# Kernel optimization log

Measured on AMD Instinct MI355X. Metric: run time of the kernel, lower is better.

Reference implementation:

```python
import jax, jax.numpy as jnp
import numpy as np

T, H, E, F, K, FS = 2048, 2048, 64, 512, 8, 512


def setup_inputs() -> dict:
    key = jax.random.key(0)
    ks = jax.random.split(key, 6)
    s = 0.02
    return {
        "hidden_states": jax.random.normal(ks[0], (T, H), jnp.float32),
        # merged gate: E router logits + 1 shared-expert gate logit
        "W_gate": jax.random.normal(ks[1], (H, E + 1), jnp.float32) * s,
        # per-expert merged gate_up proj: [E, H, 2F]
        "W_gate_up": jax.random.normal(ks[2], (E, H, 2 * F), jnp.float32) * s,
        "W_down": jax.random.normal(ks[3], (E, F, H), jnp.float32) * s,
        # shared expert
        "Ws_gate_up": jax.random.normal(ks[4], (H, 2 * FS), jnp.float32) * s,
        "Ws_down": jax.random.normal(ks[5], (FS, H), jnp.float32) * s,
    }


def reference(hidden_states, W_gate, W_gate_up, W_down, Ws_gate_up, Ws_down):
    x = hidden_states  # [T, H]
    logits_all = x @ W_gate                      # [T, E+1]
    router_logits = logits_all[:, :E]
    shared_gate_logit = logits_all[:, E:]        # [T, 1]

    # FusedMoE routing: softmax -> top_k -> renormalize (norm_topk_prob=True)
    probs = jax.nn.softmax(router_logits.astype(jnp.float32), axis=-1)
    topk_w, topk_idx = jax.lax.top_k(probs, K)   # [T, K]
    topk_w = topk_w / jnp.sum(topk_w, axis=-1, keepdims=True)
    # dense combine weights [T, E] (zero for unselected experts)
    combine = jnp.zeros((T, E), probs.dtype).at[
        jnp.arange(T)[:, None], topk_idx].set(topk_w)

    # grouped expert GEMMs (dense reference: every expert sees all tokens,
    # combine-weights zero-out unrouted pairs)
    gu = jnp.einsum('th,ehf->etf', x, W_gate_up)   # [E, T, 2F]
    g, u = jnp.split(gu, 2, axis=-1)
    act = jax.nn.silu(g) * u                       # [E, T, F]
    # apply combine weight before down-proj to avoid [E, T, H] intermediate
    act = act * combine.T[:, :, None].astype(act.dtype)
    routed = jnp.einsum('etf,efh->th', act, W_down)  # [T, H]

    # shared expert (Qwen3NextMLP with sigmoid expert_gate)
    sgu = x @ Ws_gate_up                           # [T, 2FS]
    sg, su = jnp.split(sgu, 2, axis=-1)
    shared = (jax.nn.silu(sg) * su) @ Ws_down      # [T, H]
    shared = jax.nn.sigmoid(shared_gate_logit) * shared

    return shared + routed.astype(x.dtype)
```

## Files before the change

### kernel.cpp

```cpp
#include <hip/hip_runtime.h>
#include <hip/hip_bf16.h>
#include <math.h>

#define T_TOK 2048
#define H_DIM 2048
#define E_NUM 64
#define F_DIM 512
#define K_TOP 8
#define FS_DIM 512
#define NROWS (T_TOK * K_TOP)

typedef __attribute__((ext_vector_type(8))) short short8v;
typedef __attribute__((ext_vector_type(4))) float f32x4;

static __device__ __forceinline__ unsigned short f2bf(float f) {
    unsigned int u = __float_as_uint(f);
    u += 0x7fff + ((u >> 16) & 1);
    return (unsigned short)(u >> 16);
}

#define BCHUNK(row, k8) ((((k8) ^ ((row) + ((row) >> 3)))) & 7)
#define ASWZ(row) (((row) + ((row) >> 3)) & 7)

typedef const unsigned int __attribute__((address_space(1))) gu32;
typedef unsigned int __attribute__((address_space(3))) lu32;
#define GLDS16(gsrc, ldst) \
    __builtin_amdgcn_global_load_lds((gu32*)(gsrc), (lu32*)(ldst), 16, 0, 0)

__global__ __launch_bounds__(256) void cvt_bf16_kernel(
    const float* __restrict__ in, unsigned short* __restrict__ out, int n8)
{
    int i = blockIdx.x * 256 + threadIdx.x;
    if (i < n8) {
        const float4* p = (const float4*)(in + (size_t)i * 8);
        float4 v0 = p[0], v1 = p[1];
        ushort4 a = make_ushort4(f2bf(v0.x), f2bf(v0.y), f2bf(v0.z), f2bf(v0.w));
        ushort4 b = make_ushort4(f2bf(v1.x), f2bf(v1.y), f2bf(v1.z), f2bf(v1.w));
        ushort4* q = (ushort4*)(out + (size_t)i * 8);
        q[0] = a; q[1] = b;
    }
}

__global__ __launch_bounds__(64) void router_kernel(
    const float* __restrict__ x, const float* __restrict__ Wg,
    int* __restrict__ topk_idx, float* __restrict__ topk_w,
    float* __restrict__ sgate, int* __restrict__ counts)
{
    const int t = blockIdx.x;
    const int lane = threadIdx.x;
    const float* xr = x + (size_t)t * H_DIM;

    float a0 = 0.f, a1 = 0.f, a2 = 0.f, a3 = 0.f;
    for (int h = 0; h < H_DIM; h += 4) {
        float4 xv = *(const float4*)&xr[h];
        a0 += xv.x * Wg[(h + 0) * 65 + lane];
        a1 += xv.y * Wg[(h + 1) * 65 + lane];
        a2 += xv.z * Wg[(h + 2) * 65 + lane];
        a3 += xv.w * Wg[(h + 3) * 65 + lane];
    }
    float logit = (a0 + a1) + (a2 + a3);

    float a64 = 0.f;
    for (int h = lane; h < H_DIM; h += 64) a64 += xr[h] * Wg[h * 65 + 64];
#pragma unroll
    for (int off = 32; off >= 1; off >>= 1) a64 += __shfl_xor(a64, off);

    float v = logit;
    float selv[K_TOP]; int seli[K_TOP];
#pragma unroll
    for (int k = 0; k < K_TOP; ++k) {
        float mv = v; int mi = lane;
#pragma unroll
        for (int off = 32; off >= 1; off >>= 1) {
            float ov = __shfl_xor(mv, off);
            int   oi = __shfl_xor(mi, off);
            if (ov > mv || (ov == mv && oi < mi)) { mv = ov; mi = oi; }
        }
        selv[k] = mv; seli[k] = mi;
        if (lane == mi) v = -INFINITY;
    }

    if (lane == 0) {
        float m = selv[0];
        float w[K_TOP]; float s = 0.f;
#pragma unroll
        for (int k = 0; k < K_TOP; ++k) { w[k] = __expf(selv[k] - m); s += w[k]; }
        float inv = 1.f / s;
#pragma unroll
        for (int k = 0; k < K_TOP; ++k) {
            topk_idx[t * K_TOP + k] = seli[k];
            topk_w[t * K_TOP + k] = w[k] * inv;
            atomicAdd(&counts[seli[k]], 1);
        }
        sgate[t] = 1.f / (1.f + __expf(-a64));
    }
}

__global__ __launch_bounds__(256) void bucket_kernel(
    const int* __restrict__ topk_idx, const float* __restrict__ topk_w,
    const int* __restrict__ counts, int* __restrict__ offsets,
    int* __restrict__ bucket_tok, float* __restrict__ bucket_w)
{
    const int e = blockIdx.x, thr = threadIdx.x;
    __shared__ int cnt[256];
    __shared__ int base_s;
    const int q0 = thr * 64;
    int c = 0;
    for (int q = 0; q < 64; ++q) c += (topk_idx[q0 + q] == e) ? 1 : 0;
    cnt[thr] = c;
    __syncthreads();
    if (thr == 0) {
        int off = 0;
        for (int i = 0; i < e; ++i) off += counts[i];
        offsets[e] = off;
        base_s = off;
        int run = 0;
        for (int i = 0; i < 256; ++i) { int tval = cnt[i]; cnt[i] = run; run += tval; }
    }
    __syncthreads();
    int pos = base_s + cnt[thr];
    for (int q = 0; q < 64; ++q) {
        int pp = q0 + q;
        if (topk_idx[pp] == e) {
            bucket_tok[pos] = pp >> 3;
            bucket_w[pos] = topk_w[pp];
            ++pos;
        }
    }
}

template<bool ROUTED>
__global__ __launch_bounds__(512, 6) void gu_mfma_kernel(
    const unsigned short* __restrict__ xb,
    const float* __restrict__ Wall,
    const int* __restrict__ counts, const int* __restrict__ offsets,
    const int* __restrict__ bucket_tok, const float* __restrict__ bucket_w,
    unsigned short* __restrict__ actout)
{
    constexpr int BM = 256;
    __shared__ __align__(16) unsigned short As[BM * 64];
    __shared__ __align__(16) unsigned short Bs[64 * 64];
    __shared__ int   toksS[BM];
    __shared__ float twsS[BM];

    const int tid  = threadIdx.x;
    const int lane = tid & 63;
    const int wid  = tid >> 6;
    const int wm = wid >> 1, wn = wid & 1;
    const int lrow = lane & 15, lhi = lane >> 4;

    int cblk, mt, ne, base;
    const float* W;
    if (ROUTED) {
        int nw = (blockIdx.x & 7) * ((int)gridDim.x >> 3) + (blockIdx.x >> 3);
        int e = nw >> 5; mt = (nw >> 4) & 1; cblk = nw & 15;
        ne = counts[e]; base = offsets[e];
        if (mt * BM >= ne) return;
        W = Wall + (size_t)e * H_DIM * (2 * F_DIM);
    } else {
        cblk = blockIdx.x; mt = blockIdx.y;
        ne = T_TOK; base = 0;
        W = Wall;
    }
    const int c0 = cblk * 32;

    const int n4 = (tid & 15) * 4;
    const int kb = (tid >> 4) * 2;
    const int n5 = n4 & 31;
    const int wcol = ((n5 < 16) ? 0 : (F_DIM - 16)) + c0 + (n4 >> 5) * 16 + n5;
    int wr_off[4];
#pragma unroll
    for (int cc = 0; cc < 4; ++cc) {
        int n = n4 + cc;
        wr_off[cc] = n * 64 + BCHUNK(n, kb >> 3) * 8 + (kb & 7);
    }
    const int rg = wn * 32 + lrow, ru = wn * 32 + 16 + lrow;
    int rdBg[2], rdBu[2];
#pragma unroll
    for (int ks = 0; ks < 2; ++ks) {
        int kc = ks * 4 + lhi;
        rdBg[ks] = rg * 64 + BCHUNK(rg, kc) * 8;
        rdBu[ks] = ru * 64 + BCHUNK(ru, kc) * 8;
    }
    int rdA[4][2];
#pragma unroll
    for (int fm = 0; fm < 4; ++fm) {
        int arow = wm * 64 + fm * 16 + lrow;
#pragma unroll
        for (int ks = 0; ks < 2; ++ks) {
            int kc = ks * 4 + lhi;
            rdA[fm][ks] = arow * 64 + (((kc ^ ASWZ(arow)) & 7) << 3);
        }
    }
    const int m0_stride = ROUTED ? (2 * BM) : ((int)gridDim.y * BM);

    for (int m0 = mt * BM; m0 < ne; m0 += m0_stride) {
        __syncthreads();
        if (tid < BM) {
            int idx = m0 + tid; bool v = idx < ne;
            if (ROUTED) {
                toksS[tid] = v ? bucket_tok[base + idx] : bucket_tok[base];
                twsS[tid]  = v ? bucket_w[base + idx] : 0.f;
            } else {
                toksS[tid] = v ? idx : (T_TOK - 1);
                twsS[tid]  = 1.f;
            }
        }
        __syncthreads();

        int asrc[4];
#pragma unroll
        for (int i = 0; i < 4; ++i) {
            int row = wid * 32 + i * 8 + (lane >> 3);
            asrc[i] = toksS[row] * H_DIM + (((lane & 7) ^ ASWZ(row)) << 3);
        }

        f32x4 acc[4][2];
#pragma unroll
        for (int i = 0; i < 4; ++i) {
            acc[i][0] = (f32x4){0.f, 0.f, 0.f, 0.f};
            acc[i][1] = (f32x4){0.f, 0.f, 0.f, 0.f};
        }

        const int NT = H_DIM / 64;
        float4 b0 = *(const float4*)&W[(size_t)kb * (2 * F_DIM) + wcol];
        float4 b1 = *(const float4*)&W[(size_t)(kb + 1) * (2 * F_DIM) + wcol];

        for (int kt = 0; kt < NT; ++kt) {
            const int k0 = kt * 64;
            __syncthreads();
#pragma unroll
            for (int i = 0; i < 4; ++i)
                GLDS16(xb + asrc[i] + k0, &As[(wid * 32 + i * 8) * 64]);
#pragma unroll
            for (int cc = 0; cc < 4; ++cc)
                *(ushort2*)&Bs[wr_off[cc]] = make_ushort2(
                    f2bf(((const float*)&b0)[cc]), f2bf(((const float*)&b1)[cc]));
            {
                int knx = (kt + 1 < NT) ? (k0 + 64) : k0;
                b0 = *(const float4*)&W[(size_t)(knx + kb) * (2 * F_DIM) + wcol];
                b1 = *(const float4*)&W[(size_t)(knx + kb + 1) * (2 * F_DIM) + wcol];
            }
            __syncthreads();
#pragma unroll
            for (int ks = 0; ks < 2; ++ks) {
                short8v bg = *(const short8v*)&Bs[rdBg[ks]];
                short8v bu = *(const short8v*)&Bs[rdBu[ks]];
#pragma unroll
                for (int fm = 0; fm < 4; ++fm) {
                    short8v af = *(const short8v*)&As[rdA[fm][ks]];
                    acc[fm][0] = __builtin_amdgcn_mfma_f32_16x16x32_bf16(af, bg, acc[fm][0], 0, 0, 0);
                    acc[fm][1] = __builtin_amdgcn_mfma_f32_16x16x32_bf16(af, bu, acc[fm][1], 0, 0, 0);
                }
            }
        }

        const int acol = c0 + wn * 16 + lrow;
#pragma unroll
        for (int fm = 0; fm < 4; ++fm) {
#pragma unroll
            for (int i = 0; i < 4; ++i) {
                int ml = wm * 64 + fm * 16 + lhi * 4 + i;
                int idx = m0 + ml;
                if (idx < ne) {
                    float gv = acc[fm][0][i], uv = acc[fm][1][i];
                    float s = gv / (1.f + __expf(-gv));
                    float val = s * uv * twsS[ml];
                    size_t orow = ROUTED ? (size_t)(base + idx) : (size_t)idx;
                    actout[orow * F_DIM + acol] = f2bf(val);
                }
            }
        }
    }
}

template<bool ROUTED>
__global__ __launch_bounds__(512, 6) void down_mfma_kernel(
    const unsigned short* __restrict__ actb,
    const float* __restrict__ Wall,
    const int* __restrict__ counts, const int* __restrict__ offsets,
    const int* __restrict__ bucket_tok, const float* __restrict__ sgate,
    float* __restrict__ out)
{
    constexpr int BM = 256;
    __shared__ __align__(16) unsigned short As[BM * 64];
    __shared__ __align__(16) unsigned short Bs[64 * 64];
    __shared__ int   toksS[BM];
    __shared__ float sgS[BM];

    const int tid  = threadIdx.x;
    const int lane = tid & 63;
    const int wid  = tid >> 6;
    const int wm = wid >> 1, wn = wid & 1;
    const int lrow = lane & 15, lhi = lane >> 4;

    int cblk, mt, ne, base;
    const float* W;
    if (ROUTED) {
        int nw = (blockIdx.x & 7) * ((int)gridDim.x >> 3) + (blockIdx.x >> 3);
        int e = nw >> 6; mt = (nw >> 5) & 1; cblk = nw & 31;
        ne = counts[e]; base = offsets[e];
        if (mt * BM >= ne) return;
        W = Wall + (size_t)e * F_DIM * H_DIM;
    } else {
        cblk = blockIdx.x; mt = blockIdx.y;
        ne = T_TOK; base = 0;
        W = Wall;
    }
    const int c0 = cblk * 64;

    const int n4 = (tid & 15) * 4;
    const int kb = (tid >> 4) * 2;
    const int wcol = c0 + n4;
    int wr_off[4];
#pragma unroll
    for (int cc = 0; cc < 4; ++cc) {
        int n = n4 + cc;
        wr_off[cc] = n * 64 + BCHUNK(n, kb >> 3) * 8 + (kb & 7);
    }
    const int r0 = wn * 32 + lrow, r1 = wn * 32 + 16 + lrow;
    int rdB0[2], rdB1[2];
#pragma unroll
    for (int ks = 0; ks < 2; ++ks) {
        int kc = ks * 4 + lhi;
        rdB0[ks] = r0 * 64 + BCHUNK(r0, kc) * 8;
        rdB1[ks] = r1 * 64 + BCHUNK(r1, kc) * 8;
    }
    int rdA[4][2];
#pragma unroll
    for (int fm = 0; fm < 4; ++fm) {
        int arow = wm * 64 + fm * 16 + lrow;
#pragma unroll
        for (int ks = 0; ks < 2; ++ks) {
            int kc = ks * 4 + lhi;
            rdA[fm][ks] = arow * 64 + (((kc ^ ASWZ(arow)) & 7) << 3);
        }
    }
    const int m0_stride = ROUTED ? (2 * BM) : ((int)gridDim.y * BM);

    for (int m0 = mt * BM; m0 < ne; m0 += m0_stride) {
        __syncthreads();
        if (tid < BM) {
            int idx = m0 + tid;
            if (ROUTED) {
                toksS[tid] = (idx < ne) ? bucket_tok[base + idx] : 0;
            } else {
                sgS[tid] = sgate[(idx < ne) ? idx : (T_TOK - 1)];
            }
        }
        __syncthreads();

        int asrc[4];
#pragma unroll
        for (int i = 0; i < 4; ++i) {
            int row = wid * 32 + i * 8 + (lane >> 3);
            int grow = ROUTED ? min(base + m0 + row, NROWS - 1)
                              : min(m0 + row, T_TOK - 1);
            asrc[i] = grow * F_DIM + (((lane & 7) ^ ASWZ(row)) << 3);
        }

        f32x4 acc[4][2];
#pragma unroll
        for (int i = 0; i < 4; ++i) {
            acc[i][0] = (f32x4){0.f, 0.f, 0.f, 0.f};
            acc[i][1] = (f32x4){0.f, 0.f, 0.f, 0.f};
        }

        const int NT = F_DIM / 64;
        float4 b0 = *(const float4*)&W[(size_t)kb * H_DIM + wcol];
        float4 b1 = *(const float4*)&W[(size_t)(kb + 1) * H_DIM + wcol];

        for (int kt = 0; kt < NT; ++kt) {
            const int k0 = kt * 64;
            __syncthreads();
#pragma unroll
            for (int i = 0; i < 4; ++i)
                GLDS16(actb + asrc[i] + k0, &As[(wid * 32 + i * 8) * 64]);
#pragma unroll
            for (int cc = 0; cc < 4; ++cc)
                *(ushort2*)&Bs[wr_off[cc]] = make_ushort2(
                    f2bf(((const float*)&b0)[cc]), f2bf(((const float*)&b1)[cc]));
            {
                int knx = (kt + 1 < NT) ? (k0 + 64) : k0;
                b0 = *(const float4*)&W[(size_t)(knx + kb) * H_DIM + wcol];
                b1 = *(const float4*)&W[(size_t)(knx + kb + 1) * H_DIM + wcol];
            }
            __syncthreads();
#pragma unroll
            for (int ks = 0; ks < 2; ++ks) {
                short8v bf0 = *(const short8v*)&Bs[rdB0[ks]];
                short8v bf1 = *(const short8v*)&Bs[rdB1[ks]];
#pragma unroll
                for (int fm = 0; fm < 4; ++fm) {
                    short8v af = *(const short8v*)&As[rdA[fm][ks]];
                    acc[fm][0] = __builtin_amdgcn_mfma_f32_16x16x32_bf16(af, bf0, acc[fm][0], 0, 0, 0);
                    acc[fm][1] = __builtin_amdgcn_mfma_f32_16x16x32_bf16(af, bf1, acc[fm][1], 0, 0, 0);
                }
            }
        }

#pragma unroll
        for (int fm = 0; fm < 4; ++fm) {
#pragma unroll
            for (int fn = 0; fn < 2; ++fn) {
                int col = c0 + wn * 32 + fn * 16 + lrow;
#pragma unroll
                for (int i = 0; i < 4; ++i) {
                    int ml = wm * 64 + fm * 16 + lhi * 4 + i;
                    int idx = m0 + ml;
                    if (idx < ne) {
                        if (ROUTED) {
                            atomicAdd(&out[(size_t)toksS[ml] * H_DIM + col], acc[fm][fn][i]);
                        } else {
                            out[(size_t)idx * H_DIM + col] = sgS[ml] * acc[fm][fn][i];
                        }
                    }
                }
            }
        }
    }
}

extern "C" void kernel_launch(void* const* d_in, const int* in_sizes, int n_in,
                              void* d_out, int out_size, void* d_ws, size_t ws_size,
                              hipStream_t stream) {
    const float* x    = (const float*)d_in[0];
    const float* Wg   = (const float*)d_in[1];
    const float* Wgu  = (const float*)d_in[2];
    const float* Wd   = (const float*)d_in[3];
    const float* Wsgu = (const float*)d_in[4];
    const float* Wsd  = (const float*)d_in[5];
    float* out = (float*)d_out;

    char* p = (char*)d_ws;
    auto alloc = [&](size_t bytes) {
        char* r = p;
        p += (bytes + 255) & ~(size_t)255;
        return r;
    };
    int*   topk_idx   = (int*)  alloc((size_t)T_TOK * K_TOP * sizeof(int));
    float* topk_w     = (float*)alloc((size_t)T_TOK * K_TOP * sizeof(float));
    float* sgate      = (float*)alloc((size_t)T_TOK * sizeof(float));
    int*   counts     = (int*)  alloc((size_t)E_NUM * sizeof(int));
    int*   offsets    = (int*)  alloc((size_t)E_NUM * sizeof(int));
    int*   bucket_tok = (int*)  alloc((size_t)NROWS * sizeof(int));
    float* bucket_w   = (float*)alloc((size_t)NROWS * sizeof(float));
    unsigned short* xb    = (unsigned short*)alloc((size_t)T_TOK * H_DIM * sizeof(short));
    unsigned short* act_r = (unsigned short*)alloc((size_t)NROWS * F_DIM * sizeof(short));
    unsigned short* act_s = (unsigned short*)alloc((size_t)T_TOK * FS_DIM * sizeof(short));

    hipMemsetAsync(counts, 0, E_NUM * sizeof(int), stream);
    cvt_bf16_kernel<<<(T_TOK * H_DIM / 8 + 255) / 256, 256, 0, stream>>>(x, xb, T_TOK * H_DIM / 8);
    router_kernel<<<T_TOK, 64, 0, stream>>>(x, Wg, topk_idx, topk_w, sgate, counts);
    bucket_kernel<<<E_NUM, 256, 0, stream>>>(topk_idx, topk_w, counts, offsets, bucket_tok, bucket_w);

    gu_mfma_kernel<true><<<16 * E_NUM * 2, 512, 0, stream>>>(
        xb, Wgu, counts, offsets, bucket_tok, bucket_w, act_r);
    gu_mfma_kernel<false><<<dim3(16, T_TOK / 256), 512, 0, stream>>>(
        xb, Wsgu, counts, offsets, bucket_tok, bucket_w, act_s);

    down_mfma_kernel<false><<<dim3(32, T_TOK / 256), 512, 0, stream>>>(
        act_s, Wsd, counts, offsets, bucket_tok, sgate, out);
    down_mfma_kernel<true><<<32 * E_NUM * 2, 512, 0, stream>>>(
        act_r, Wd, counts, offsets, bucket_tok, sgate, out);
}
```

Before: 819.7 us.

## Double-buffer A and B LDS tiles in grouped MoE GEMMs with K-32 stages

Splits the K loop of both the gate-up and down MFMA kernels into 32-wide stages with ping-pong LDS buffers for A and B. The global-to-LDS load of the next stage is issued before the MFMAs of the current one, leaving one barrier per stage instead of two per 64-wide tile. The A tile swizzle changes to fit 32-column rows. This adds LDS use (A split in half but B doubled) and more barriers in total, which may affect occupancy.

```diff
diff --git a/kernel.cpp b/kernel.cpp
--- a/kernel.cpp
+++ b/kernel.cpp
@@ -20,7 +20,7 @@
 }
 
 #define BCHUNK(row, k8) ((((k8) ^ ((row) + ((row) >> 3)))) & 7)
-#define ASWZ(row) (((row) + ((row) >> 3)) & 7)
+#define ASW32(r) (((r) >> 1) & 3)
 
 typedef const unsigned int __attribute__((address_space(1))) gu32;
 typedef unsigned int __attribute__((address_space(3))) lu32;
@@ -138,8 +138,8 @@
     unsigned short* __restrict__ actout)
 {
     constexpr int BM = 256;
-    __shared__ __align__(16) unsigned short As[BM * 64];
-    __shared__ __align__(16) unsigned short Bs[64 * 64];
+    __shared__ __align__(16) unsigned short As[2][BM * 32];
+    __shared__ __align__(16) unsigned short Bs[2][64 * 64];
     __shared__ int   toksS[BM];
     __shared__ float twsS[BM];
 
@@ -182,16 +182,16 @@
         rdBg[ks] = rg * 64 + BCHUNK(rg, kc) * 8;
         rdBu[ks] = ru * 64 + BCHUNK(ru, kc) * 8;
     }
-    int rdA[4][2];
+    int rdA[4];
 #pragma unroll
     for (int fm = 0; fm < 4; ++fm) {
         int arow = wm * 64 + fm * 16 + lrow;
-#pragma unroll
-        for (int ks = 0; ks < 2; ++ks) {
-            int kc = ks * 4 + lhi;
-            rdA[fm][ks] = arow * 64 + (((kc ^ ASWZ(arow)) & 7) << 3);
-        }
-    }
+        rdA[fm] = arow * 32 + ((lhi ^ ASW32(arow)) << 3);
+    }
+    const int ar0 = wid * 32 + (lane >> 2);
+    const int ar1 = ar0 + 16;
+    const int NT   = H_DIM / 64;
+    const int SMAX = H_DIM / 32;
     const int m0_stride = ROUTED ? (2 * BM) : ((int)gridDim.y * BM);
 
     for (int m0 = mt * BM; m0 < ne; m0 += m0_stride) {
@@ -208,12 +208,8 @@
         }
         __syncthreads();
 
-        int asrc[4];
-#pragma unroll
-        for (int i = 0; i < 4; ++i) {
-            int row = wid * 32 + i * 8 + (lane >> 3);
-            asrc[i] = toksS[row] * H_DIM + (((lane & 7) ^ ASWZ(row)) << 3);
-        }
+        const int src0 = toksS[ar0] * H_DIM + (((lane & 3) ^ ASW32(ar0)) << 3);
+        const int src1 = toksS[ar1] * H_DIM + (((lane & 3) ^ ASW32(ar1)) << 3);
 
         f32x4 acc[4][2];
 #pragma unroll
@@ -222,37 +218,47 @@
             acc[i][1] = (f32x4){0.f, 0.f, 0.f, 0.f};
         }
 
-        const int NT = H_DIM / 64;
         float4 b0 = *(const float4*)&W[(size_t)kb * (2 * F_DIM) + wcol];
         float4 b1 = *(const float4*)&W[(size_t)(kb + 1) * (2 * F_DIM) + wcol];
-
-        for (int kt = 0; kt < NT; ++kt) {
-            const int k0 = kt * 64;
-            __syncthreads();
-#pragma unroll
-            for (int i = 0; i < 4; ++i)
-                GLDS16(xb + asrc[i] + k0, &As[(wid * 32 + i * 8) * 64]);
-#pragma unroll
-            for (int cc = 0; cc < 4; ++cc)
-                *(ushort2*)&Bs[wr_off[cc]] = make_ushort2(
-                    f2bf(((const float*)&b0)[cc]), f2bf(((const float*)&b1)[cc]));
-            {
-                int knx = (kt + 1 < NT) ? (k0 + 64) : k0;
+        GLDS16(xb + src0, &As[0][(wid * 32) * 32]);
+        GLDS16(xb + src1, &As[0][(wid * 32 + 16) * 32]);
+#pragma unroll
+        for (int cc = 0; cc < 4; ++cc)
+            *(ushort2*)&Bs[0][wr_off[cc]] = make_ushort2(
+                f2bf(((const float*)&b0)[cc]), f2bf(((const float*)&b1)[cc]));
+        b0 = *(const float4*)&W[(size_t)(64 + kb) * (2 * F_DIM) + wcol];
+        b1 = *(const float4*)&W[(size_t)(64 + kb + 1) * (2 * F_DIM) + wcol];
+        __syncthreads();
+
+        for (int s = 0; s < SMAX; ++s) {
+            const int kt = s >> 1;
+            if (s + 1 < SMAX) {
+                const int kof = (s + 1) * 32;
+                GLDS16(xb + src0 + kof, &As[(s + 1) & 1][(wid * 32) * 32]);
+                GLDS16(xb + src1 + kof, &As[(s + 1) & 1][(wid * 32 + 16) * 32]);
+            }
+            if ((s & 1) && (kt + 1 < NT)) {
+#pragma unroll
+                for (int cc = 0; cc < 4; ++cc)
+                    *(ushort2*)&Bs[(kt + 1) & 1][wr_off[cc]] = make_ushort2(
+                        f2bf(((const float*)&b0)[cc]), f2bf(((const float*)&b1)[cc]));
+                int knx = (kt + 2 < NT) ? (kt + 2) * 64 : (NT - 1) * 64;
                 b0 = *(const float4*)&W[(size_t)(knx + kb) * (2 * F_DIM) + wcol];
                 b1 = *(const float4*)&W[(size_t)(knx + kb + 1) * (2 * F_DIM) + wcol];
             }
+            __builtin_amdgcn_sched_barrier(0);
+            const unsigned short* A_ = As[s & 1];
+            const unsigned short* B_ = Bs[kt & 1];
+            const int ks = s & 1;
+            short8v bg = *(const short8v*)&B_[rdBg[ks]];
+            short8v bu = *(const short8v*)&B_[rdBu[ks]];
+#pragma unroll
+            for (int fm = 0; fm < 4; ++fm) {
+                short8v af = *(const short8v*)&A_[rdA[fm]];
+                acc[fm][0] = __builtin_amdgcn_mfma_f32_16x16x32_bf16(af, bg, acc[fm][0], 0, 0, 0);
+                acc[fm][1] = __builtin_amdgcn_mfma_f32_16x16x32_bf16(af, bu, acc[fm][1], 0, 0, 0);
+            }
             __syncthreads();
-#pragma unroll
-            for (int ks = 0; ks < 2; ++ks) {
-                short8v bg = *(const short8v*)&Bs[rdBg[ks]];
-                short8v bu = *(const short8v*)&Bs[rdBu[ks]];
-#pragma unroll
-                for (int fm = 0; fm < 4; ++fm) {
-                    short8v af = *(const short8v*)&As[rdA[fm][ks]];
-                    acc[fm][0] = __builtin_amdgcn_mfma_f32_16x16x32_bf16(af, bg, acc[fm][0], 0, 0, 0);
-                    acc[fm][1] = __builtin_amdgcn_mfma_f32_16x16x32_bf16(af, bu, acc[fm][1], 0, 0, 0);
-                }
-            }
         }
 
         const int acol = c0 + wn * 16 + lrow;
@@ -283,8 +289,8 @@
     float* __restrict__ out)
 {
     constexpr int BM = 256;
-    __shared__ __align__(16) unsigned short As[BM * 64];
-    __shared__ __align__(16) unsigned short Bs[64 * 64];
+    __shared__ __align__(16) unsigned short As[2][BM * 32];
+    __shared__ __align__(16) unsigned short Bs[2][64 * 64];
     __shared__ int   toksS[BM];
     __shared__ float sgS[BM];
 
@@ -326,16 +332,16 @@
         rdB0[ks] = r0 * 64 + BCHUNK(r0, kc) * 8;
         rdB1[ks] = r1 * 64 + BCHUNK(r1, kc) * 8;
     }
-    int rdA[4][2];
+    int rdA[4];
 #pragma unroll
     for (int fm = 0; fm < 4; ++fm) {
         int arow = wm * 64 + fm * 16 + lrow;
-#pragma unroll
-        for (int ks = 0; ks < 2; ++ks) {
-            int kc = ks * 4 + lhi;
-            rdA[fm][ks] = arow * 64 + (((kc ^ ASWZ(arow)) & 7) << 3);
-        }
-    }
+        rdA[fm] = arow * 32 + ((lhi ^ ASW32(arow)) << 3);
+    }
+    const int ar0 = wid * 32 + (lane >> 2);
+    const int ar1 = ar0 + 16;
+    const int NT   = F_DIM / 64;
+    const int SMAX = F_DIM / 32;
     const int m0_stride = ROUTED ? (2 * BM) : ((int)gridDim.y * BM);
 
     for (int m0 = mt * BM; m0 < ne; m0 += m0_stride) {
@@ -350,14 +356,10 @@
         }
         __syncthreads();
 
-        int asrc[4];
-#pragma unroll
-        for (int i = 0; i < 4; ++i) {
-            int row = wid * 32 + i * 8 + (lane >> 3);
-            int grow = ROUTED ? min(base + m0 + row, NROWS - 1)
-                              : min(m0 + row, T_TOK - 1);
-            asrc[i] = grow * F_DIM + (((lane & 7) ^ ASWZ(row)) << 3);
-        }
+        int g0 = ROUTED ? min(base + m0 + ar0, NROWS - 1) : min(m0 + ar0, T_TOK - 1);
+        int g1 = ROUTED ? min(base + m0 + ar1, NROWS - 1) : min(m0 + ar1, T_TOK - 1);
+        const int src0 = g0 * F_DIM + (((lane & 3) ^ ASW32(ar0)) << 3);
+        const int src1 = g1 * F_DIM + (((lane & 3) ^ ASW32(ar1)) << 3);
 
         f32x4 acc[4][2];
 #pragma unroll
@@ -366,37 +368,47 @@
             acc[i][1] = (f32x4){0.f, 0.f, 0.f, 0.f};
         }
 
-        const int NT = F_DIM / 64;
         float4 b0 = *(const float4*)&W[(size_t)kb * H_DIM + wcol];
         float4 b1 = *(const float4*)&W[(size_t)(kb + 1) * H_DIM + wcol];
-
-        for (int kt = 0; kt < NT; ++kt) {
-            const int k0 = kt * 64;
-            __syncthreads();
-#pragma unroll
-            for (int i = 0; i < 4; ++i)
-                GLDS16(actb + asrc[i] + k0, &As[(wid * 32 + i * 8) * 64]);
-#pragma unroll
-            for (int cc = 0; cc < 4; ++cc)
-                *(ushort2*)&Bs[wr_off[cc]] = make_ushort2(
-                    f2bf(((const float*)&b0)[cc]), f2bf(((const float*)&b1)[cc]));
-            {
-                int knx = (kt + 1 < NT) ? (k0 + 64) : k0;
+        GLDS16(actb + src0, &As[0][(wid * 32) * 32]);
+        GLDS16(actb + src1, &As[0][(wid * 32 + 16) * 32]);
+#pragma unroll
+        for (int cc = 0; cc < 4; ++cc)
+            *(ushort2*)&Bs[0][wr_off[cc]] = make_ushort2(
+                f2bf(((const float*)&b0)[cc]), f2bf(((const float*)&b1)[cc]));
+        b0 = *(const float4*)&W[(size_t)(64 + kb) * H_DIM + wcol];
+        b1 = *(const float4*)&W[(size_t)(64 + kb + 1) * H_DIM + wcol];
+        __syncthreads();
+
+        for (int s = 0; s < SMAX; ++s) {
+            const int kt = s >> 1;
+            if (s + 1 < SMAX) {
+                const int kof = (s + 1) * 32;
+                GLDS16(actb + src0 + kof, &As[(s + 1) & 1][(wid * 32) * 32]);
+                GLDS16(actb + src1 + kof, &As[(s + 1) & 1][(wid * 32 + 16) * 32]);
+            }
+            if ((s & 1) && (kt + 1 < NT)) {
+#pragma unroll
+                for (int cc = 0; cc < 4; ++cc)
+                    *(ushort2*)&Bs[(kt + 1) & 1][wr_off[cc]] = make_ushort2(
+                        f2bf(((const float*)&b0)[cc]), f2bf(((const float*)&b1)[cc]));
+                int knx = (kt + 2 < NT) ? (kt + 2) * 64 : (NT - 1) * 64;
                 b0 = *(const float4*)&W[(size_t)(knx + kb) * H_DIM + wcol];
                 b1 = *(const float4*)&W[(size_t)(knx + kb + 1) * H_DIM + wcol];
             }
+            __builtin_amdgcn_sched_barrier(0);
+            const unsigned short* A_ = As[s & 1];
+            const unsigned short* B_ = Bs[kt & 1];
+            const int ks = s & 1;
+            short8v bf0 = *(const short8v*)&B_[rdB0[ks]];
+            short8v bf1 = *(const short8v*)&B_[rdB1[ks]];
+#pragma unroll
+            for (int fm = 0; fm < 4; ++fm) {
+                short8v af = *(const short8v*)&A_[rdA[fm]];
+                acc[fm][0] = __builtin_amdgcn_mfma_f32_16x16x32_bf16(af, bf0, acc[fm][0], 0, 0, 0);
+                acc[fm][1] = __builtin_amdgcn_mfma_f32_16x16x32_bf16(af, bf1, acc[fm][1], 0, 0, 0);
+            }
             __syncthreads();
-#pragma unroll
-            for (int ks = 0; ks < 2; ++ks) {
-                short8v bf0 = *(const short8v*)&Bs[rdB0[ks]];
-                short8v bf1 = *(const short8v*)&Bs[rdB1[ks]];
-#pragma unroll
-                for (int fm = 0; fm < 4; ++fm) {
-                    short8v af = *(const short8v*)&As[rdA[fm][ks]];
-                    acc[fm][0] = __builtin_amdgcn_mfma_f32_16x16x32_bf16(af, bf0, acc[fm][0], 0, 0, 0);
-                    acc[fm][1] = __builtin_amdgcn_mfma_f32_16x16x32_bf16(af, bf1, acc[fm][1], 0, 0, 0);
-                }
-            }
         }
 
 #pragma unroll
```

Measured after the change: 745.4 us. 9.1% less time.

## Load A fragments directly from global and double-buffer B tile in LDS

Applied to the files above, without the earlier changes.

The A operand (tokens/activations) no longer goes through LDS via global_load_lds; each lane loads its MFMA fragments straight from global memory into registers, prefetched one half-step ahead. The B weight tile becomes double-buffered in LDS so one barrier per k-step suffices, and launch bounds drop occupancy to 4 waves/SIMD. The routed grids also stop splitting experts into two M-tiles, so each block loops over all of its expert's rows. This targets barrier stalls and LDS traffic, at the cost of uncoalesced 16-byte gathers of A, less parallelism for experts with many tokens, and reordered launch of the shared gate-up kernel.

```diff
diff --git a/kernel.cpp b/kernel.cpp
--- a/kernel.cpp
+++ b/kernel.cpp
@@ -20,12 +20,11 @@
 }
 
 #define BCHUNK(row, k8) ((((k8) ^ ((row) + ((row) >> 3)))) & 7)
-#define ASWZ(row) (((row) + ((row) >> 3)) & 7)
-
-typedef const unsigned int __attribute__((address_space(1))) gu32;
-typedef unsigned int __attribute__((address_space(3))) lu32;
-#define GLDS16(gsrc, ldst) \
-    __builtin_amdgcn_global_load_lds((gu32*)(gsrc), (lu32*)(ldst), 16, 0, 0)
+
+#define PIPE_BARRIER() do { \
+    asm volatile("s_waitcnt lgkmcnt(0)" ::: "memory"); \
+    __builtin_amdgcn_s_barrier(); \
+} while (0)
 
 __global__ __launch_bounds__(256) void cvt_bf16_kernel(
     const float* __restrict__ in, unsigned short* __restrict__ out, int n8)
@@ -130,7 +129,7 @@
 }
 
 template<bool ROUTED>
-__global__ __launch_bounds__(512, 6) void gu_mfma_kernel(
+__global__ __launch_bounds__(512, 4) void gu_mfma_kernel(
     const unsigned short* __restrict__ xb,
     const float* __restrict__ Wall,
     const int* __restrict__ counts, const int* __restrict__ offsets,
@@ -138,8 +137,7 @@
     unsigned short* __restrict__ actout)
 {
     constexpr int BM = 256;
-    __shared__ __align__(16) unsigned short As[BM * 64];
-    __shared__ __align__(16) unsigned short Bs[64 * 64];
+    __shared__ __align__(16) unsigned short Bs[2][64 * 64];
     __shared__ int   toksS[BM];
     __shared__ float twsS[BM];
 
@@ -149,16 +147,15 @@
     const int wm = wid >> 1, wn = wid & 1;
     const int lrow = lane & 15, lhi = lane >> 4;
 
-    int cblk, mt, ne, base;
+    int cblk, ne, base;
     const float* W;
     if (ROUTED) {
         int nw = (blockIdx.x & 7) * ((int)gridDim.x >> 3) + (blockIdx.x >> 3);
-        int e = nw >> 5; mt = (nw >> 4) & 1; cblk = nw & 15;
+        int e = nw >> 4; cblk = nw & 15;
         ne = counts[e]; base = offsets[e];
-        if (mt * BM >= ne) return;
         W = Wall + (size_t)e * H_DIM * (2 * F_DIM);
     } else {
-        cblk = blockIdx.x; mt = blockIdx.y;
+        cblk = blockIdx.x;
         ne = T_TOK; base = 0;
         W = Wall;
     }
@@ -175,26 +172,19 @@
         wr_off[cc] = n * 64 + BCHUNK(n, kb >> 3) * 8 + (kb & 7);
     }
     const int rg = wn * 32 + lrow, ru = wn * 32 + 16 + lrow;
-    int rdBg[2], rdBu[2];
+    int rd_g[2], rd_u[2];
 #pragma unroll
     for (int ks = 0; ks < 2; ++ks) {
         int kc = ks * 4 + lhi;
-        rdBg[ks] = rg * 64 + BCHUNK(rg, kc) * 8;
-        rdBu[ks] = ru * 64 + BCHUNK(ru, kc) * 8;
-    }
-    int rdA[4][2];
-#pragma unroll
-    for (int fm = 0; fm < 4; ++fm) {
-        int arow = wm * 64 + fm * 16 + lrow;
-#pragma unroll
-        for (int ks = 0; ks < 2; ++ks) {
-            int kc = ks * 4 + lhi;
-            rdA[fm][ks] = arow * 64 + (((kc ^ ASWZ(arow)) & 7) << 3);
-        }
-    }
-    const int m0_stride = ROUTED ? (2 * BM) : ((int)gridDim.y * BM);
-
-    for (int m0 = mt * BM; m0 < ne; m0 += m0_stride) {
+        rd_g[ks] = rg * 64 + BCHUNK(rg, kc) * 8;
+        rd_u[ks] = ru * 64 + BCHUNK(ru, kc) * 8;
+    }
+
+    const int m0_beg = ROUTED ? 0 : blockIdx.y * BM;
+    const int m0_end = ROUTED ? ne : m0_beg + BM;
+    const int NT = H_DIM / 64;
+
+    for (int m0 = m0_beg; m0 < m0_end; m0 += BM) {
         __syncthreads();
         if (tid < BM) {
             int idx = m0 + tid; bool v = idx < ne;
@@ -208,11 +198,11 @@
         }
         __syncthreads();
 
-        int asrc[4];
-#pragma unroll
-        for (int i = 0; i < 4; ++i) {
-            int row = wid * 32 + i * 8 + (lane >> 3);
-            asrc[i] = toksS[row] * H_DIM + (((lane & 7) ^ ASWZ(row)) << 3);
+        const unsigned short* aptr[4];
+#pragma unroll
+        for (int fm = 0; fm < 4; ++fm) {
+            int r = wm * 64 + fm * 16 + lrow;
+            aptr[fm] = xb + (size_t)toksS[r] * H_DIM;
         }
 
         f32x4 acc[4][2];
@@ -222,37 +212,64 @@
             acc[i][1] = (f32x4){0.f, 0.f, 0.f, 0.f};
         }
 
-        const int NT = H_DIM / 64;
         float4 b0 = *(const float4*)&W[(size_t)kb * (2 * F_DIM) + wcol];
         float4 b1 = *(const float4*)&W[(size_t)(kb + 1) * (2 * F_DIM) + wcol];
+#pragma unroll
+        for (int cc = 0; cc < 4; ++cc)
+            *(ushort2*)&Bs[0][wr_off[cc]] = make_ushort2(
+                f2bf(((const float*)&b0)[cc]), f2bf(((const float*)&b1)[cc]));
+        b0 = *(const float4*)&W[(size_t)(64 + kb) * (2 * F_DIM) + wcol];
+        b1 = *(const float4*)&W[(size_t)(64 + kb + 1) * (2 * F_DIM) + wcol];
+        short8v afp[4];
+#pragma unroll
+        for (int fm = 0; fm < 4; ++fm)
+            afp[fm] = *(const short8v*)(aptr[fm] + lhi * 8);
+        PIPE_BARRIER();
 
         for (int kt = 0; kt < NT; ++kt) {
             const int k0 = kt * 64;
-            __syncthreads();
-#pragma unroll
-            for (int i = 0; i < 4; ++i)
-                GLDS16(xb + asrc[i] + k0, &As[(wid * 32 + i * 8) * 64]);
-#pragma unroll
-            for (int cc = 0; cc < 4; ++cc)
-                *(ushort2*)&Bs[wr_off[cc]] = make_ushort2(
-                    f2bf(((const float*)&b0)[cc]), f2bf(((const float*)&b1)[cc]));
-            {
-                int knx = (kt + 1 < NT) ? (k0 + 64) : k0;
+            if (kt + 1 < NT) {
+                unsigned short* nB = Bs[(kt + 1) & 1];
+#pragma unroll
+                for (int cc = 0; cc < 4; ++cc)
+                    *(ushort2*)&nB[wr_off[cc]] = make_ushort2(
+                        f2bf(((const float*)&b0)[cc]), f2bf(((const float*)&b1)[cc]));
+                int knx = (kt + 2 < NT) ? (k0 + 128) : (k0 + 64);
                 b0 = *(const float4*)&W[(size_t)(knx + kb) * (2 * F_DIM) + wcol];
                 b1 = *(const float4*)&W[(size_t)(knx + kb + 1) * (2 * F_DIM) + wcol];
             }
-            __syncthreads();
-#pragma unroll
-            for (int ks = 0; ks < 2; ++ks) {
-                short8v bg = *(const short8v*)&Bs[rdBg[ks]];
-                short8v bu = *(const short8v*)&Bs[rdBu[ks]];
+            short8v af1[4];
+#pragma unroll
+            for (int fm = 0; fm < 4; ++fm)
+                af1[fm] = *(const short8v*)(aptr[fm] + k0 + (4 + lhi) * 8);
+            __builtin_amdgcn_sched_barrier(0);
+            {
+                const unsigned short* B_ = Bs[kt & 1];
+                short8v bg = *(const short8v*)&B_[rd_g[0]];
+                short8v bu = *(const short8v*)&B_[rd_u[0]];
 #pragma unroll
                 for (int fm = 0; fm < 4; ++fm) {
-                    short8v af = *(const short8v*)&As[rdA[fm][ks]];
-                    acc[fm][0] = __builtin_amdgcn_mfma_f32_16x16x32_bf16(af, bg, acc[fm][0], 0, 0, 0);
-                    acc[fm][1] = __builtin_amdgcn_mfma_f32_16x16x32_bf16(af, bu, acc[fm][1], 0, 0, 0);
+                    acc[fm][0] = __builtin_amdgcn_mfma_f32_16x16x32_bf16(afp[fm], bg, acc[fm][0], 0, 0, 0);
+                    acc[fm][1] = __builtin_amdgcn_mfma_f32_16x16x32_bf16(afp[fm], bu, acc[fm][1], 0, 0, 0);
                 }
             }
+            if (kt + 1 < NT) {
+#pragma unroll
+                for (int fm = 0; fm < 4; ++fm)
+                    afp[fm] = *(const short8v*)(aptr[fm] + k0 + 64 + lhi * 8);
+            }
+            __builtin_amdgcn_sched_barrier(0);
+            {
+                const unsigned short* B_ = Bs[kt & 1];
+                short8v bg = *(const short8v*)&B_[rd_g[1]];
+                short8v bu = *(const short8v*)&B_[rd_u[1]];
+#pragma unroll
+                for (int fm = 0; fm < 4; ++fm) {
+                    acc[fm][0] = __builtin_amdgcn_mfma_f32_16x16x32_bf16(af1[fm], bg, acc[fm][0], 0, 0, 0);
+                    acc[fm][1] = __builtin_amdgcn_mfma_f32_16x16x32_bf16(af1[fm], bu, acc[fm][1], 0, 0, 0);
+                }
+            }
+            PIPE_BARRIER();
         }
 
         const int acol = c0 + wn * 16 + lrow;
@@ -275,7 +292,7 @@
 }
 
 template<bool ROUTED>
-__global__ __launch_bounds__(512, 6) void down_mfma_kernel(
+__global__ __launch_bounds__(512, 4) void down_mfma_kernel(
     const unsigned short* __restrict__ actb,
     const float* __restrict__ Wall,
     const int* __restrict__ counts, const int* __restrict__ offsets,
@@ -283,8 +300,7 @@
     float* __restrict__ out)
 {
     constexpr int BM = 256;
-    __shared__ __align__(16) unsigned short As[BM * 64];
-    __shared__ __align__(16) unsigned short Bs[64 * 64];
+    __shared__ __align__(16) unsigned short Bs[2][64 * 64];
     __shared__ int   toksS[BM];
     __shared__ float sgS[BM];
 
@@ -294,16 +310,15 @@
     const int wm = wid >> 1, wn = wid & 1;
     const int lrow = lane & 15, lhi = lane >> 4;
 
-    int cblk, mt, ne, base;
+    int cblk, ne, base;
     const float* W;
     if (ROUTED) {
         int nw = (blockIdx.x & 7) * ((int)gridDim.x >> 3) + (blockIdx.x >> 3);
-        int e = nw >> 6; mt = (nw >> 5) & 1; cblk = nw & 31;
+        int e = nw >> 5; cblk = nw & 31;
         ne = counts[e]; base = offsets[e];
-        if (mt * BM >= ne) return;
         W = Wall + (size_t)e * F_DIM * H_DIM;
     } else {
-        cblk = blockIdx.x; mt = blockIdx.y;
+        cblk = blockIdx.x;
         ne = T_TOK; base = 0;
         W = Wall;
     }
@@ -319,26 +334,19 @@
         wr_off[cc] = n * 64 + BCHUNK(n, kb >> 3) * 8 + (kb & 7);
     }
     const int r0 = wn * 32 + lrow, r1 = wn * 32 + 16 + lrow;
-    int rdB0[2], rdB1[2];
+    int rd_0[2], rd_1[2];
 #pragma unroll
     for (int ks = 0; ks < 2; ++ks) {
         int kc = ks * 4 + lhi;
-        rdB0[ks] = r0 * 64 + BCHUNK(r0, kc) * 8;
-        rdB1[ks] = r1 * 64 + BCHUNK(r1, kc) * 8;
-    }
-    int rdA[4][2];
-#pragma unroll
-    for (int fm = 0; fm < 4; ++fm) {
-        int arow = wm * 64 + fm * 16 + lrow;
-#pragma unroll
-        for (int ks = 0; ks < 2; ++ks) {
-            int kc = ks * 4 + lhi;
-            rdA[fm][ks] = arow * 64 + (((kc ^ ASWZ(arow)) & 7) << 3);
-        }
-    }
-    const int m0_stride = ROUTED ? (2 * BM) : ((int)gridDim.y * BM);
-
-    for (int m0 = mt * BM; m0 < ne; m0 += m0_stride) {
+        rd_0[ks] = r0 * 64 + BCHUNK(r0, kc) * 8;
+        rd_1[ks] = r1 * 64 + BCHUNK(r1, kc) * 8;
+    }
+
+    const int m0_beg = ROUTED ? 0 : blockIdx.y * BM;
+    const int m0_end = ROUTED ? ne : m0_beg + BM;
+    const int NT = F_DIM / 64;
+
+    for (int m0 = m0_beg; m0 < m0_end; m0 += BM) {
         __syncthreads();
         if (tid < BM) {
             int idx = m0 + tid;
@@ -350,13 +358,12 @@
         }
         __syncthreads();
 
-        int asrc[4];
-#pragma unroll
-        for (int i = 0; i < 4; ++i) {
-            int row = wid * 32 + i * 8 + (lane >> 3);
-            int grow = ROUTED ? min(base + m0 + row, NROWS - 1)
-                              : min(m0 + row, T_TOK - 1);
-            asrc[i] = grow * F_DIM + (((lane & 7) ^ ASWZ(row)) << 3);
+        const unsigned short* aptr[4];
+#pragma unroll
+        for (int fm = 0; fm < 4; ++fm) {
+            int r = wm * 64 + fm * 16 + lrow;
+            int grow = ROUTED ? min(base + m0 + r, NROWS - 1) : min(m0 + r, T_TOK - 1);
+            aptr[fm] = actb + (size_t)grow * F_DIM;
         }
 
         f32x4 acc[4][2];
@@ -366,37 +373,64 @@
             acc[i][1] = (f32x4){0.f, 0.f, 0.f, 0.f};
         }
 
-        const int NT = F_DIM / 64;
         float4 b0 = *(const float4*)&W[(size_t)kb * H_DIM + wcol];
         float4 b1 = *(const float4*)&W[(size_t)(kb + 1) * H_DIM + wcol];
+#pragma unroll
+        for (int cc = 0; cc < 4; ++cc)
+            *(ushort2*)&Bs[0][wr_off[cc]] = make_ushort2(
+                f2bf(((const float*)&b0)[cc]), f2bf(((const float*)&b1)[cc]));
+        b0 = *(const float4*)&W[(size_t)(64 + kb) * H_DIM + wcol];
+        b1 = *(const float4*)&W[(size_t)(64 + kb + 1) * H_DIM + wcol];
+        short8v afp[4];
+#pragma unroll
+        for (int fm = 0; fm < 4; ++fm)
+            afp[fm] = *(const short8v*)(aptr[fm] + lhi * 8);
+        PIPE_BARRIER();
 
         for (int kt = 0; kt < NT; ++kt) {
             const int k0 = kt * 64;
-            __syncthreads();
-#pragma unroll
-            for (int i = 0; i < 4; ++i)
-                GLDS16(actb + asrc[i] + k0, &As[(wid * 32 + i * 8) * 64]);
-#pragma unroll
-            for (int cc = 0; cc < 4; ++cc)
-                *(ushort2*)&Bs[wr_off[cc]] = make_ushort2(
-                    f2bf(((const float*)&b0)[cc]), f2bf(((const float*)&b1)[cc]));
-            {
-                int knx = (kt + 1 < NT) ? (k0 + 64) : k0;
+            if (kt + 1 < NT) {
+                unsigned short* nB = Bs[(kt + 1) & 1];
+#pragma unroll
+                for (int cc = 0; cc < 4; ++cc)
+                    *(ushort2*)&nB[wr_off[cc]] = make_ushort2(
+                        f2bf(((const float*)&b0)[cc]), f2bf(((const float*)&b1)[cc]));
+                int knx = (kt + 2 < NT) ? (k0 + 128) : (k0 + 64);
                 b0 = *(const float4*)&W[(size_t)(knx + kb) * H_DIM + wcol];
                 b1 = *(const float4*)&W[(size_t)(knx + kb + 1) * H_DIM + wcol];
             }
-            __syncthreads();
-#pragma unroll
-            for (int ks = 0; ks < 2; ++ks) {
-                short8v bf0 = *(const short8v*)&Bs[rdB0[ks]];
-                short8v bf1 = *(const short8v*)&Bs[rdB1[ks]];
+            short8v af1[4];
+#pragma unroll
+            for (int fm = 0; fm < 4; ++fm)
+                af1[fm] = *(const short8v*)(aptr[fm] + k0 + (4 + lhi) * 8);
+            __builtin_amdgcn_sched_barrier(0);
+            {
+                const unsigned short* B_ = Bs[kt & 1];
+                short8v bf0 = *(const short8v*)&B_[rd_0[0]];
+                short8v bf1 = *(const short8v*)&B_[rd_1[0]];
 #pragma unroll
                 for (int fm = 0; fm < 4; ++fm) {
-                    short8v af = *(const short8v*)&As[rdA[fm][ks]];
-                    acc[fm][0] = __builtin_amdgcn_mfma_f32_16x16x32_bf16(af, bf0, acc[fm][0], 0, 0, 0);
-                    acc[fm][1] = __builtin_amdgcn_mfma_f32_16x16x32_bf16(af, bf1, acc[fm][1], 0, 0, 0);
+                    acc[fm][0] = __builtin_amdgcn_mfma_f32_16x16x32_bf16(afp[fm], bf0, acc[fm][0], 0, 0, 0);
+                    acc[fm][1] = __builtin_amdgcn_mfma_f32_16x16x32_bf16(afp[fm], bf1, acc[fm][1], 0, 0, 0);
                 }
             }
+            if (kt + 1 < NT) {
+#pragma unroll
+                for (int fm = 0; fm < 4; ++fm)
+                    afp[fm] = *(const short8v*)(aptr[fm] + k0 + 64 + lhi * 8);
+            }
+            __builtin_amdgcn_sched_barrier(0);
+            {
+                const unsigned short* B_ = Bs[kt & 1];
+                short8v bf0 = *(const short8v*)&B_[rd_0[1]];
+                short8v bf1 = *(const short8v*)&B_[rd_1[1]];
+#pragma unroll
+                for (int fm = 0; fm < 4; ++fm) {
+                    acc[fm][0] = __builtin_amdgcn_mfma_f32_16x16x32_bf16(af1[fm], bf0, acc[fm][0], 0, 0, 0);
+                    acc[fm][1] = __builtin_amdgcn_mfma_f32_16x16x32_bf16(af1[fm], bf1, acc[fm][1], 0, 0, 0);
+                }
+            }
+            PIPE_BARRIER();
         }
 
 #pragma unroll
@@ -454,13 +488,13 @@
     router_kernel<<<T_TOK, 64, 0, stream>>>(x, Wg, topk_idx, topk_w, sgate, counts);
     bucket_kernel<<<E_NUM, 256, 0, stream>>>(topk_idx, topk_w, counts, offsets, bucket_tok, bucket_w);
 
-    gu_mfma_kernel<true><<<16 * E_NUM * 2, 512, 0, stream>>>(
-        xb, Wgu, counts, offsets, bucket_tok, bucket_w, act_r);
     gu_mfma_kernel<false><<<dim3(16, T_TOK / 256), 512, 0, stream>>>(
         xb, Wsgu, counts, offsets, bucket_tok, bucket_w, act_s);
+    gu_mfma_kernel<true><<<16 * E_NUM, 512, 0, stream>>>(
+        xb, Wgu, counts, offsets, bucket_tok, bucket_w, act_r);
 
     down_mfma_kernel<false><<<dim3(32, T_TOK / 256), 512, 0, stream>>>(
         act_s, Wsd, counts, offsets, bucket_tok, sgate, out);
-    down_mfma_kernel<true><<<32 * E_NUM * 2, 512, 0, stream>>>(
+    down_mfma_kernel<true><<<32 * E_NUM, 512, 0, stream>>>(
         act_r, Wd, counts, offsets, bucket_tok, sgate, out);
 }
```

Result: slower. 971.8 us (+18.6%).
